# Kernel optimization log

Hardware: AMD Instinct MI355X
Metric: run time of the kernel (lower is better)

Reference implementation:

```python
import jax, jax.numpy as jnp
import numpy as np


def _patchify(x, p):
    # x: [B, V, H, W] -> [B, V, L, p*p] with L = (H/p)*(W/p), matching Conv2d(kernel=stride=p)
    B, V, H, W = x.shape
    hp, wp = H // p, W // p
    x = x.reshape(B, V, hp, p, wp, p)
    x = x.transpose(0, 1, 2, 4, 3, 5)  # [B, V, hp, wp, p, p]
    return x.reshape(B, V, hp * wp, p * p)


def setup_inputs() -> dict:
    key = jax.random.key(0)
    ks = jax.random.split(key, 12)
    B, V, H, W, p, D = 2, 16, 128, 256, 4, 1024
    L = (H // p) * (W // p)  # 2048
    std = 0.02
    return {
        "x": jax.random.normal(ks[0], (B, V, H, W), jnp.float32),
        "proj_w": jax.random.normal(ks[1], (V, D, p * p), jnp.float32) * std,
        "proj_b": jnp.zeros((V, D), jnp.float32),
        "channel_embed": jax.random.normal(ks[2], (1, V, D), jnp.float32) * std,
        "pos_embed": jax.random.normal(ks[3], (1, L, D), jnp.float32) * std,
        "channel_query": jax.random.normal(ks[4], (1, 1, D), jnp.float32) * std,
        "wq": jax.random.normal(ks[5], (D, D), jnp.float32) * std,
        "wk": jax.random.normal(ks[6], (D, D), jnp.float32) * std,
        "wv": jax.random.normal(ks[7], (D, D), jnp.float32) * std,
        "bq": jnp.zeros((D,), jnp.float32),
        "bk": jnp.zeros((D,), jnp.float32),
        "bv": jnp.zeros((D,), jnp.float32),
        "wo": jax.random.normal(ks[8], (D, D), jnp.float32) * std,
        "bo": jnp.zeros((D,), jnp.float32),
        "num_heads": 16,
    }


def reference(x, proj_w, proj_b, channel_embed, pos_embed, channel_query,
              wq, wk, wv, bq, bk, bv, wo, bo, num_heads):
    D = proj_w.shape[1]
    p = int(round(np.sqrt(proj_w.shape[-1])))
    nh = int(num_heads)
    dh = D // nh

    # per-variable patch embed (Conv2d k=stride=p == patch-matmul)
    patches = _patchify(x, p)                                   # [B, V, L, p*p]
    tok = jnp.einsum('bvlk,vdk->bvld', patches, proj_w)         # [B, V, L, D]
    tok = tok + proj_b[None, :, None, :]

    # add variable (channel) and positional embeddings
    tok = tok + channel_embed[:, :, None, :] + pos_embed[:, None, :, :]

    # aggregate_variables: single-query MHA over V, batched over B*L
    h = tok.transpose(0, 2, 1, 3)                               # [B, L, V, D]
    q = channel_query[0, 0] @ wq.T + bq                         # [D]
    qh = q.reshape(nh, dh)
    k = (jnp.einsum('blvd,ed->blve', h, wk) + bk).reshape(*h.shape[:3], nh, dh)
    v = (jnp.einsum('blvd,ed->blve', h, wv) + bv).reshape(*h.shape[:3], nh, dh)
    scores = jnp.einsum('he,blvhe->blhv', qh, k) / np.sqrt(dh)  # [B, L, nh, V]
    attn = jax.nn.softmax(scores, axis=-1)
    ctx = jnp.einsum('blhv,blvhe->blhe', attn, v)               # [B, L, nh, dh]
    ctx = ctx.reshape(h.shape[0], h.shape[1], D)
    out = ctx @ wo.T + bo                                       # [B, L, D]
    return out
```

## Files before the change

### kernel.cpp

```cpp
#include <hip/hip_runtime.h>
#include <hip/hip_bf16.h>

using bf16 = __hip_bfloat16;
using bf16x8 = __attribute__((ext_vector_type(8))) short;
using f32x4  = __attribute__((ext_vector_type(4))) float;

__device__ inline unsigned short f2bu(float f){ bf16 h = __float2bfloat16(f); return *(unsigned short*)&h; }
__device__ inline void async_cp16(const void* g, void* l){
  __builtin_amdgcn_global_load_lds((const __attribute__((address_space(1))) void*)g,
                                   (__attribute__((address_space(3))) void*)l, 16, 0, 0);
}
union BF8 { unsigned short s[8]; bf16x8 v; };

constexpr int D_ = 1024, L_ = 2048;
constexpr int CN = 384;
constexpr int WBS = 288;

__global__ __launch_bounds__(256) void k_prep2(const float* __restrict__ wv, const float* __restrict__ wo,
                                               const float* __restrict__ pe,
                                               const float* __restrict__ proj_w, const float* __restrict__ proj_b,
                                               const float* __restrict__ ce, const float* __restrict__ cq,
                                               const float* __restrict__ wq, const float* __restrict__ bq,
                                               const float* __restrict__ wk,
                                               unsigned short* __restrict__ Ab, unsigned short* __restrict__ wo_b,
                                               unsigned short* __restrict__ pe_b,
                                               unsigned short* __restrict__ Btb){
  __shared__ float t[64][17];
  __shared__ float qL[64];
  __shared__ float red[4][64];
  const int blk = blockIdx.x;
  const int tid = threadIdx.x;
  if (blk < 4096){
    int i = blk*256 + tid;
    const float* src; unsigned short* dst; size_t off;
    if (i < 262144){ src = wv; dst = Ab;   off = i; }
    else if (i < 524288){ src = wo; dst = wo_b; off = i - 262144; }
    else           { src = pe; dst = pe_b; off = i - 524288; }
    float4 v = *(const float4*)(src + off*4);
    *(ushort4*)(dst + off*4) = make_ushort4(f2bu(v.x), f2bu(v.y), f2bu(v.z), f2bu(v.w));
  } else if (blk < 4352){
    const int r_ = blk - 4096;
    const int v = r_ >> 4, dd0 = (r_ & 15)*64;
    { const int r = tid >> 2, kq = tid & 3;
      float4 a = *(const float4*)(proj_w + ((size_t)(v*D_ + dd0 + r))*16 + kq*4);
      t[r][kq*4+0]=a.x; t[r][kq*4+1]=a.y; t[r][kq*4+2]=a.z; t[r][kq*4+3]=a.w; }
    __syncthreads();
    { const int k = tid >> 4, c0 = (tid & 15)*4;
      ushort4 o = make_ushort4(f2bu(t[c0+0][k]), f2bu(t[c0+1][k]), f2bu(t[c0+2][k]), f2bu(t[c0+3][k]));
      *(ushort4*)(Btb + (size_t)(v*16+k)*D_ + dd0 + c0) = o; }
    if (tid < 16){
      const int c0 = tid*4;
      float4 pb = *(const float4*)(proj_b + v*D_ + dd0 + c0);
      float4 cc = *(const float4*)(ce     + v*D_ + dd0 + c0);
      ushort4 o = make_ushort4(f2bu(pb.x+cc.x), f2bu(pb.y+cc.y), f2bu(pb.z+cc.z), f2bu(pb.w+cc.w));
      *(ushort4*)(Btb + (size_t)(256+v)*D_ + dd0 + c0) = o;
    }
  } else {
    const int b = blk - 4352;
    const int hh = b >> 4, dq = b & 15;
    const int wave = tid >> 6, lane = tid & 63;
    {
      float cqv[16];
      #pragma unroll
      for (int k=0;k<16;++k) cqv[k] = cq[lane + 64*k];
      #pragma unroll
      for (int j=0;j<16;++j){
        const int e = hh*64 + wave*16 + j;
        const float* wr = wq + (size_t)e*D_;
        float p = 0.f;
        #pragma unroll
        for (int k=0;k<16;++k) p += cqv[k]*wr[lane + 64*k];
        #pragma unroll
        for (int m=32;m>=1;m>>=1) p += __shfl_xor(p, m, 64);
        if (lane==0) qL[wave*16+j] = p + bq[e];
      }
    }
    __syncthreads();
    {
      const int eg = wave, dl = lane;
      const int d = dq*64 + dl;
      float s = 0.f;
      #pragma unroll
      for (int j=0;j<16;++j){
        int e = hh*64 + eg*16 + j;
        s += qL[eg*16+j]*wk[(size_t)e*D_ + d];
      }
      red[eg][dl] = s;
      __syncthreads();
      if (eg==0)
        Ab[(size_t)(1024+hh)*D_ + d] = f2bu(((red[0][dl]+red[1][dl]) + (red[2][dl]+red[3][dl]))*0.125f);
    }
  }
}

template<int MFRAG, bool BIAS, bool WB2>
__device__ inline void gemm_body(unsigned short* As, unsigned short* Bs,
                                 const unsigned short* __restrict__ Abf, const unsigned short* __restrict__ Bt,
                                 const float* __restrict__ bias, float* __restrict__ C,
                                 unsigned short* __restrict__ W, const float* __restrict__ bvp,
                                 int m0, int n0, int K, int ldc, int Mvalid){
  const int tid = threadIdx.x;
  const int wave = tid >> 6, lane = tid & 63;
  const int wm = wave & 1, wn = wave >> 1;
  const int lm = lane & 15, kg4 = lane >> 4;
  f32x4 acc[MFRAG][4];
  #pragma unroll
  for (int mf=0;mf<MFRAG;++mf)
    #pragma unroll
    for (int nf=0;nf<4;++nf) acc[mf][nf] = (f32x4){0.f,0.f,0.f,0.f};
  for (int k0=0; k0<K; k0+=64){
    #pragma unroll
    for (int i=0;i<MFRAG;++i){
      int idx = i*256 + tid;
      int row = idx >> 3, g = (idx & 7) ^ (row & 7);
      async_cp16(Abf + (size_t)(m0+row)*K + k0 + g*8, &As[idx*8]);
    }
    #pragma unroll
    for (int i=0;i<4;++i){
      int idx = i*256 + tid;
      int row = idx >> 3, g = (idx & 7) ^ (row & 7);
      async_cp16(Bt + (size_t)(n0+row)*K + k0 + g*8, &Bs[idx*8]);
    }
    __syncthreads();
    #pragma unroll
    for (int c=0;c<2;++c){
      bf16x8 af[MFRAG], bfr[4];
      #pragma unroll
      for (int f=0;f<MFRAG;++f){
        int row = wm*16*MFRAG + f*16 + lm;
        af[f] = *(const bf16x8*)(&As[row*64 + (((c*4+kg4) ^ (row&7)))*8]);
      }
      #pragma unroll
      for (int f=0;f<4;++f){
        int colr = wn*64 + f*16 + lm;
        bfr[f] = *(const bf16x8*)(&Bs[colr*64 + (((c*4+kg4) ^ (colr&7)))*8]);
      }
      #pragma unroll
      for (int mf=0;mf<MFRAG;++mf)
        #pragma unroll
        for (int nf=0;nf<4;++nf)
          acc[mf][nf] = __builtin_amdgcn_mfma_f32_16x16x32_bf16(af[mf], bfr[nf], acc[mf][nf], 0,0,0);
    }
    __syncthreads();
  }
  #pragma unroll
  for (int nf=0;nf<4;++nf){
    int col = n0 + wn*64 + nf*16 + lm;
    float bval = BIAS ? bias[col] : 0.f;
    #pragma unroll
    for (int mf=0;mf<MFRAG;++mf){
      #pragma unroll
      for (int r=0;r<4;++r){
        int row = m0 + wm*16*MFRAG + mf*16 + kg4*4 + r;
        if (row < Mvalid){
          float v = acc[mf][nf][r];
          C[(size_t)row*ldc + col] = v + bval;
          if (WB2 && row < 1024){
            if (col < 256)      W[(size_t)row*WBS + col] = f2bu(v);
            else if (col < 272) W[(size_t)row*WBS + col] = f2bu(v + bvp[row]);
            else if (col < 288) W[(size_t)row*WBS + col] = 0;
          }
        }
      }
    }
  }
}

__global__ __launch_bounds__(256) void k_gemmCP2(const unsigned short* __restrict__ Ab,
                                                 const unsigned short* __restrict__ Btb,
                                                 const unsigned short* __restrict__ pe_b,
                                                 const float* __restrict__ bv,
                                                 float* __restrict__ Cbig, unsigned short* __restrict__ Wb2,
                                                 float* __restrict__ P2){
  __shared__ unsigned short As[64*64];
  __shared__ unsigned short Bs[128*64];
  if (blockIdx.x < 51){
    int bx = blockIdx.x % 3, by = blockIdx.x / 3;
    gemm_body<2,false,true>(As, Bs, Ab, Btb, nullptr, Cbig, Wb2, bv, by*64, bx*128, 1024, CN, 1040);
  } else {
    int b = blockIdx.x - 51;
    int bx = b & 7, by = b >> 3;
    gemm_body<1,false,false>(As, Bs, pe_b, Ab, nullptr, P2, nullptr, nullptr, by*32, bx*128, 1024, 1024, 2048);
  }
}

__global__ __launch_bounds__(256) void k_gemmOut(const unsigned short* __restrict__ ctxF,
                                                 const unsigned short* __restrict__ wo_b,
                                                 const float* __restrict__ bo, float* __restrict__ C){
  __shared__ unsigned short As[64*64];
  __shared__ unsigned short Bs[128*64];
  gemm_body<2,true,false>(As, Bs, ctxF, wo_b, bo, C, nullptr, nullptr,
                          blockIdx.y*64, blockIdx.x*128, 1024, 1024, 4096);
}

__global__ __launch_bounds__(256) void k_fused8(const float* __restrict__ x,
                                                const float* __restrict__ Cbig,
                                                const unsigned short* __restrict__ Wb2,
                                                const float* __restrict__ P2,
                                                unsigned short* __restrict__ ctxF){
  __shared__ float patchP[16*260];
  __shared__ float attnT[4*320];
  const int tid = threadIdx.x;
  const int bb  = blockIdx.x >> 9;
  const int sg  = (blockIdx.x >> 2) & 127;
  const int hqq = blockIdx.x & 3;
  unsigned short* ctx = ctxF + (size_t)bb*L_*D_;
  const int l0 = sg*16;
  {
    const int v = tid >> 4, u = tid & 15;
    const int hi = l0 >> 6, wi0 = l0 & 63;
    const float* xp = x + ((size_t)((bb*16+v)*128 + hi*4)*256 + (wi0+u)*4);
    float* dst = &patchP[u*260 + v*16];
    #pragma unroll
    for (int pi=0; pi<4; ++pi){
      float4 r = *(const float4*)(xp + pi*256);
      dst[pi*4+0]=r.x; dst[pi*4+1]=r.y; dst[pi*4+2]=r.z; dst[pi*4+3]=r.w;
    }
  }
  __syncthreads();
  if (tid < 64){
    const int s = tid >> 2, h4 = tid & 3;
    const int hh = hqq*4 + h4;
    const float* qrow = Cbig + (size_t)(1024+hh)*CN;
    const float* prow = &patchP[s*260];
    float4 qc0 = *(const float4*)(qrow+256);
    float4 qc1 = *(const float4*)(qrow+260);
    float4 qc2 = *(const float4*)(qrow+264);
    float4 qc3 = *(const float4*)(qrow+268);
    float qcv[16] = {qc0.x,qc0.y,qc0.z,qc0.w, qc1.x,qc1.y,qc1.z,qc1.w,
                     qc2.x,qc2.y,qc2.z,qc2.w, qc3.x,qc3.y,qc3.z,qc3.w};
    float sc[16];
    #pragma unroll
    for (int v=0; v<16; ++v){
      const float* qp = qrow + v*16;
      const float* pp = prow + v*16;
      float4 qa = *(const float4*)(qp+0),  qb = *(const float4*)(qp+4);
      float4 qc = *(const float4*)(qp+8),  qd = *(const float4*)(qp+12);
      float4 pa = *(const float4*)(pp+0),  pb2 = *(const float4*)(pp+4);
      float4 pc = *(const float4*)(pp+8),  pd = *(const float4*)(pp+12);
      float a = qcv[v];
      a += qa.x*pa.x + qa.y*pa.y + qa.z*pa.z + qa.w*pa.w;
      a += qb.x*pb2.x + qb.y*pb2.y + qb.z*pb2.z + qb.w*pb2.w;
      a += qc.x*pc.x + qc.y*pc.y + qc.z*pc.z + qc.w*pc.w;
      a += qd.x*pd.x + qd.y*pd.y + qd.z*pd.z + qd.w*pd.w;
      sc[v] = a;
    }
    float mx = sc[0];
    #pragma unroll
    for (int v=1;v<16;++v) mx = fmaxf(mx, sc[v]);
    float sum = 0.f;
    #pragma unroll
    for (int v=0;v<16;++v){ sc[v] = __expf(sc[v]-mx); sum += sc[v]; }
    float inv = 1.f/sum;
    float* arow = &attnT[h4*320 + s*20];
    #pragma unroll
    for (int v=0;v<16;++v) arow[v] = sc[v]*inv;
  }
  __syncthreads();
  const int wave = tid >> 6, lane = tid & 63;
  const int m = lane & 15, quad = lane >> 4;
  const int hh = hqq*4 + wave;
  const float* at = &attnT[wave*320];
  f32x4 acc[4];
  #pragma unroll
  for (int dt=0;dt<4;++dt) acc[dt] = (f32x4){0.f,0.f,0.f,0.f};
  #pragma unroll
  for (int vp=0; vp<9; ++vp){
    BF8 af;
    if (vp < 8){
      const int v = vp*2 + (quad>>1);
      const int k8 = (quad&1)*8;
      const float aw = at[m*20 + v];
      const float* pp = &patchP[m*260 + v*16 + k8];
      float4 p0 = *(const float4*)(pp+0);
      float4 p1 = *(const float4*)(pp+4);
      af.s[0]=f2bu(aw*p0.x); af.s[1]=f2bu(aw*p0.y); af.s[2]=f2bu(aw*p0.z); af.s[3]=f2bu(aw*p0.w);
      af.s[4]=f2bu(aw*p1.x); af.s[5]=f2bu(aw*p1.y); af.s[6]=f2bu(aw*p1.z); af.s[7]=f2bu(aw*p1.w);
    } else {
      #pragma unroll
      for (int j=0;j<8;++j)
        af.s[j] = (quad < 2) ? f2bu(at[m*20 + quad*8 + j]) : (unsigned short)0;
    }
    #pragma unroll
    for (int dt=0; dt<4; ++dt){
      const int d = hh*64 + dt*16 + m;
      const bf16x8 bf = *(const bf16x8*)(Wb2 + (size_t)d*WBS + vp*32 + quad*8);
      acc[dt] = __builtin_amdgcn_mfma_f32_16x16x32_bf16(af.v, bf, acc[dt], 0,0,0);
    }
  }
  #pragma unroll
  for (int dt=0; dt<4; ++dt){
    const int d = hh*64 + dt*16 + m;
    #pragma unroll
    for (int r=0;r<4;++r){
      const int s = quad*4 + r;
      ctx[(size_t)(l0+s)*D_ + d] = f2bu(acc[dt][r] + P2[(size_t)(l0+s)*D_ + d]);
    }
  }
}

extern "C" void kernel_launch(void* const* d_in, const int* in_sizes, int n_in,
                              void* d_out, int out_size, void* d_ws, size_t ws_size,
                              hipStream_t stream){
  const float* x      = (const float*)d_in[0];
  const float* proj_w = (const float*)d_in[1];
  const float* proj_b = (const float*)d_in[2];
  const float* ce     = (const float*)d_in[3];
  const float* pe     = (const float*)d_in[4];
  const float* cq     = (const float*)d_in[5];
  const float* wq     = (const float*)d_in[6];
  const float* wk     = (const float*)d_in[7];
  const float* wv     = (const float*)d_in[8];
  const float* bq     = (const float*)d_in[9];
  const float* bv     = (const float*)d_in[11];
  const float* wo     = (const float*)d_in[12];
  const float* bo     = (const float*)d_in[13];
  float* out = (float*)d_out;

  char* base = (char*)d_ws;
  unsigned short* Ab   = (unsigned short*)(base);
  unsigned short* Btb  = (unsigned short*)(base + 2359296);
  float*          Cbig = (float*)(base + 3145728);
  unsigned short* wo_b = (unsigned short*)(base + 4743168);
  unsigned short* Wb2  = (unsigned short*)(base + 6840320);
  float*          P2   = (float*)(base + 7430144);
  unsigned short* ctxF = (unsigned short*)(base + 15818752);
  unsigned short* pe_b = (unsigned short*)(base + 24207360);

  k_prep2<<<4608, 256, 0, stream>>>(wv, wo, pe, proj_w, proj_b, ce, cq, wq, bq, wk, Ab, wo_b, pe_b, Btb);
  k_gemmCP2<<<563, 256, 0, stream>>>(Ab, Btb, pe_b, bv, Cbig, Wb2, P2);
  k_fused8<<<1024, 256, 0, stream>>>(x, Cbig, Wb2, P2, ctxF);
  k_gemmOut<<<dim3(8,64), 256, 0, stream>>>(ctxF, wo_b, bo, out);
}
```

Measured before the change: 175.4 us.

## Double-buffer GEMM LDS tiles with async prefetch and vmcnt waits

Converts the shared GEMM body from single-buffered load-then-compute into a two-stage pipeline. The next K-tile is issued via global_load_lds into the alternate buffer while the current one is consumed, with explicit s_waitcnt vmcnt counts and raw s_barrier replacing __syncthreads. The goal is to hide global-to-LDS latency behind MFMA work in both the fused projection GEMM and the output GEMM. LDS use doubles to 48KB per block, which may reduce occupancy. The hand-coded vmcnt thresholds must match the number of outstanding loads per stage.

```diff
diff --git a/kernel.cpp b/kernel.cpp
--- a/kernel.cpp
+++ b/kernel.cpp
@@ -9,6 +9,11 @@
 __device__ inline void async_cp16(const void* g, void* l){
   __builtin_amdgcn_global_load_lds((const __attribute__((address_space(1))) void*)g,
                                    (__attribute__((address_space(3))) void*)l, 16, 0, 0);
+}
+template<int N> __device__ inline void wait_vmcnt(){
+  if constexpr (N==0)      asm volatile("s_waitcnt vmcnt(0)" ::: "memory");
+  else if constexpr (N==5) asm volatile("s_waitcnt vmcnt(5)" ::: "memory");
+  else if constexpr (N==6) asm volatile("s_waitcnt vmcnt(6)" ::: "memory");
 }
 union BF8 { unsigned short s[8]; bf16x8 v; };
 
@@ -103,37 +108,53 @@
   const int wave = tid >> 6, lane = tid & 63;
   const int wm = wave & 1, wn = wave >> 1;
   const int lm = lane & 15, kg4 = lane >> 4;
+  constexpr int ASZ = MFRAG*32*64;
+  constexpr int BSZ = 128*64;
+  constexpr int NLD = MFRAG + 4;
   f32x4 acc[MFRAG][4];
   #pragma unroll
   for (int mf=0;mf<MFRAG;++mf)
     #pragma unroll
     for (int nf=0;nf<4;++nf) acc[mf][nf] = (f32x4){0.f,0.f,0.f,0.f};
-  for (int k0=0; k0<K; k0+=64){
+
+  auto stage = [&](int t, int buf){
+    const int k0 = t << 6;
     #pragma unroll
     for (int i=0;i<MFRAG;++i){
       int idx = i*256 + tid;
       int row = idx >> 3, g = (idx & 7) ^ (row & 7);
-      async_cp16(Abf + (size_t)(m0+row)*K + k0 + g*8, &As[idx*8]);
+      async_cp16(Abf + (size_t)(m0+row)*K + k0 + g*8, &As[buf*ASZ + idx*8]);
     }
     #pragma unroll
     for (int i=0;i<4;++i){
       int idx = i*256 + tid;
       int row = idx >> 3, g = (idx & 7) ^ (row & 7);
-      async_cp16(Bt + (size_t)(n0+row)*K + k0 + g*8, &Bs[idx*8]);
-    }
-    __syncthreads();
+      async_cp16(Bt + (size_t)(n0+row)*K + k0 + g*8, &Bs[buf*BSZ + idx*8]);
+    }
+  };
+
+  const int NT = K >> 6;
+  stage(0, 0);
+  for (int t=0; t<NT; ++t){
+    const int cur = t & 1;
+    if (t+1 < NT){ stage(t+1, cur^1); wait_vmcnt<NLD>(); }
+    else         { wait_vmcnt<0>(); }
+    __builtin_amdgcn_s_barrier();
+    __builtin_amdgcn_sched_barrier(0);
+    const unsigned short* Asc = &As[cur*ASZ];
+    const unsigned short* Bsc = &Bs[cur*BSZ];
     #pragma unroll
     for (int c=0;c<2;++c){
       bf16x8 af[MFRAG], bfr[4];
       #pragma unroll
       for (int f=0;f<MFRAG;++f){
         int row = wm*16*MFRAG + f*16 + lm;
-        af[f] = *(const bf16x8*)(&As[row*64 + (((c*4+kg4) ^ (row&7)))*8]);
+        af[f] = *(const bf16x8*)(&Asc[row*64 + (((c*4+kg4) ^ (row&7)))*8]);
       }
       #pragma unroll
       for (int f=0;f<4;++f){
         int colr = wn*64 + f*16 + lm;
-        bfr[f] = *(const bf16x8*)(&Bs[colr*64 + (((c*4+kg4) ^ (colr&7)))*8]);
+        bfr[f] = *(const bf16x8*)(&Bsc[colr*64 + (((c*4+kg4) ^ (colr&7)))*8]);
       }
       #pragma unroll
       for (int mf=0;mf<MFRAG;++mf)
@@ -141,7 +162,8 @@
         for (int nf=0;nf<4;++nf)
           acc[mf][nf] = __builtin_amdgcn_mfma_f32_16x16x32_bf16(af[mf], bfr[nf], acc[mf][nf], 0,0,0);
     }
-    __syncthreads();
+    __builtin_amdgcn_sched_barrier(0);
+    __builtin_amdgcn_s_barrier();
   }
   #pragma unroll
   for (int nf=0;nf<4;++nf){
@@ -172,8 +194,8 @@
                                                  const float* __restrict__ bv,
                                                  float* __restrict__ Cbig, unsigned short* __restrict__ Wb2,
                                                  float* __restrict__ P2){
-  __shared__ unsigned short As[64*64];
-  __shared__ unsigned short Bs[128*64];
+  __shared__ unsigned short As[2*64*64];
+  __shared__ unsigned short Bs[2*128*64];
   if (blockIdx.x < 51){
     int bx = blockIdx.x % 3, by = blockIdx.x / 3;
     gemm_body<2,false,true>(As, Bs, Ab, Btb, nullptr, Cbig, Wb2, bv, by*64, bx*128, 1024, CN, 1040);
@@ -187,8 +209,8 @@
 __global__ __launch_bounds__(256) void k_gemmOut(const unsigned short* __restrict__ ctxF,
                                                  const unsigned short* __restrict__ wo_b,
                                                  const float* __restrict__ bo, float* __restrict__ C){
-  __shared__ unsigned short As[64*64];
-  __shared__ unsigned short Bs[128*64];
+  __shared__ unsigned short As[2*64*64];
+  __shared__ unsigned short Bs[2*128*64];
   gemm_body<2,true,false>(As, Bs, ctxF, wo_b, bo, C, nullptr, nullptr,
                           blockIdx.y*64, blockIdx.x*128, 1024, 1024, 4096);
 }
```

After: 180.7 us. 1.03x slower.

## Pre-swizzle value weights into MFMA fragment order and stage ctx stores through LDS

Applied to the files above, without the earlier changes.

The GEMM epilogue now writes the bf16 value-projection weights in an order that matches the MFMA B-fragment layout, one contiguous block per head. Each wave's loads in the fused attention kernel therefore become fully coalesced 16-byte-per-lane reads instead of row-strided ones. The bf16 context output is also staged in shared memory and written back as 32-byte contiguous chunks per thread, replacing scattered 2-byte stores. This costs an extra LDS buffer, one extra barrier, and more scattered writes in the GEMM epilogue.

```diff
diff --git a/kernel.cpp b/kernel.cpp
--- a/kernel.cpp
+++ b/kernel.cpp
@@ -14,7 +14,12 @@
 
 constexpr int D_ = 1024, L_ = 2048;
 constexpr int CN = 384;
-constexpr int WBS = 288;
+
+__device__ inline size_t w3idx(int row, int col){
+  const int hh = row >> 6, m = row & 15, dt = (row >> 4) & 3;
+  const int vp = col >> 5, quad = (col >> 3) & 3, j = col & 7;
+  return (size_t)hh*18432 + vp*2048 + dt*512 + quad*128 + m*8 + j;
+}
 
 __global__ __launch_bounds__(256) void k_prep2(const float* __restrict__ wv, const float* __restrict__ wo,
                                                const float* __restrict__ pe,
@@ -156,9 +161,9 @@
           float v = acc[mf][nf][r];
           C[(size_t)row*ldc + col] = v + bval;
           if (WB2 && row < 1024){
-            if (col < 256)      W[(size_t)row*WBS + col] = f2bu(v);
-            else if (col < 272) W[(size_t)row*WBS + col] = f2bu(v + bvp[row]);
-            else if (col < 288) W[(size_t)row*WBS + col] = 0;
+            if (col < 256)      W[w3idx(row,col)] = f2bu(v);
+            else if (col < 272) W[w3idx(row,col)] = f2bu(v + bvp[row]);
+            else if (col < 288) W[w3idx(row,col)] = 0;
           }
         }
       }
@@ -193,13 +198,14 @@
                           blockIdx.y*64, blockIdx.x*128, 1024, 1024, 4096);
 }
 
-__global__ __launch_bounds__(256) void k_fused8(const float* __restrict__ x,
+__global__ __launch_bounds__(256) void k_fused9(const float* __restrict__ x,
                                                 const float* __restrict__ Cbig,
-                                                const unsigned short* __restrict__ Wb2,
+                                                const unsigned short* __restrict__ W3,
                                                 const float* __restrict__ P2,
                                                 unsigned short* __restrict__ ctxF){
   __shared__ float patchP[16*260];
   __shared__ float attnT[4*320];
+  __shared__ __align__(16) unsigned short S[16*264];
   const int tid = threadIdx.x;
   const int bb  = blockIdx.x >> 9;
   const int sg  = (blockIdx.x >> 2) & 127;
@@ -261,6 +267,7 @@
   const int m = lane & 15, quad = lane >> 4;
   const int hh = hqq*4 + wave;
   const float* at = &attnT[wave*320];
+  const unsigned short* wbase = W3 + (size_t)hh*18432 + lane*8;
   f32x4 acc[4];
   #pragma unroll
   for (int dt=0;dt<4;++dt) acc[dt] = (f32x4){0.f,0.f,0.f,0.f};
@@ -283,19 +290,27 @@
     }
     #pragma unroll
     for (int dt=0; dt<4; ++dt){
-      const int d = hh*64 + dt*16 + m;
-      const bf16x8 bf = *(const bf16x8*)(Wb2 + (size_t)d*WBS + vp*32 + quad*8);
+      const bf16x8 bf = *(const bf16x8*)(wbase + vp*2048 + dt*512);
       acc[dt] = __builtin_amdgcn_mfma_f32_16x16x32_bf16(af.v, bf, acc[dt], 0,0,0);
     }
   }
+  const int dblk0 = wave*64;
   #pragma unroll
   for (int dt=0; dt<4; ++dt){
-    const int d = hh*64 + dt*16 + m;
+    const int d = hqq*256 + dblk0 + dt*16 + m;
     #pragma unroll
     for (int r=0;r<4;++r){
       const int s = quad*4 + r;
-      ctx[(size_t)(l0+s)*D_ + d] = f2bu(acc[dt][r] + P2[(size_t)(l0+s)*D_ + d]);
-    }
+      S[s*264 + dblk0 + dt*16 + m] = f2bu(acc[dt][r] + P2[(size_t)(l0+s)*D_ + d]);
+    }
+  }
+  __syncthreads();
+  {
+    const int row = tid >> 4, ch = tid & 15;
+    const unsigned short* srcp = &S[row*264 + ch*16];
+    unsigned short* dstp = ctx + (size_t)(l0+row)*D_ + hqq*256 + ch*16;
+    *(uint4*)(dstp)   = *(const uint4*)(srcp);
+    *(uint4*)(dstp+8) = *(const uint4*)(srcp+8);
   }
 }
 
@@ -329,6 +344,6 @@
 
   k_prep2<<<4608, 256, 0, stream>>>(wv, wo, pe, proj_w, proj_b, ce, cq, wq, bq, wk, Ab, wo_b, pe_b, Btb);
   k_gemmCP2<<<563, 256, 0, stream>>>(Ab, Btb, pe_b, bv, Cbig, Wb2, P2);
-  k_fused8<<<1024, 256, 0, stream>>>(x, Cbig, Wb2, P2, ctxF);
+  k_fused9<<<1024, 256, 0, stream>>>(x, Cbig, Wb2, P2, ctxF);
   k_gemmOut<<<dim3(8,64), 256, 0, stream>>>(ctxF, wo_b, bo, out);
 }
```

After: 173.8 us. About the same (-0.9%).
